# Performance work log

Measured on AMD Instinct MI355X. Metric: run time of the kernel, lower is better.

The kernel has to match this reference:

```python
import jax, jax.numpy as jnp
import numpy as np

CMIN, CMAX = -1024.0, 1016.0  # clamp(min=-2**10, max=2**10 - 8) after every op
BRIGHT_F = 1.9   # 1.0 + linspace(0, 0.9, 11)[10]
COLOR_F = 1.9    # 1.0 + linspace(0, 0.9, 11)[10]


def _brightness_dct(x, f):
    # pixel-domain multiplicative brightness; DCT is linear -> scale all coeffs
    return x * f


def _contrast_dct(x, f):
    # pixel contrast: (p - mean)*f + mean.
    # In DCT: AC coeffs scale by f; DC coeff blends toward per-channel mean DC.
    dc_mean = jnp.mean(x[..., 0, 0], axis=(-2, -1), keepdims=True)  # [C,1,1]
    out = x * f
    out = out.at[..., 0, 0].add((1.0 - f) * dc_mean)
    return out


def setup_inputs() -> dict:
    key = jax.random.key(0)
    k1, k2 = jax.random.split(key)
    # luma: [C=1, Hblocks, Wblocks, 8, 8]; chroma 4:2:0: [C=2, H/2, W/2, 8, 8]
    y = jax.random.normal(k1, (1, 512, 512, 8, 8), dtype=jnp.float32) * 100.0
    c = jax.random.normal(k2, (2, 256, 256, 8, 8), dtype=jnp.float32) * 100.0
    return {"y": y, "c": c}


def reference(y, c):
    clamp = lambda t: jnp.clip(t, CMIN, CMAX)
    # dct_prep(mode='start') treated as identity; initial clamp as in forward()
    y = clamp(y)
    c = clamp(c)
    # op 1: Brightness on luma (coeff[0]); both planes clamped after each op
    y = clamp(_brightness_dct(y, BRIGHT_F))
    c = clamp(c)
    # op 2: Color = contrast on chroma (coeff[1])
    c = clamp(_contrast_dct(c, COLOR_F))
    y = clamp(y)
    # dct_prep(mode='end') treated as identity
    return y, c
```

## Files before the change

### kernel.cpp

```cpp
#include <hip/hip_runtime.h>

#define CMIN -1024.0f
#define CMAX 1016.0f

__device__ __forceinline__ float clampv(float x) {
    return fminf(fmaxf(x, CMIN), CMAX);
}

__global__ void __launch_bounds__(256)
dc_sum_kernel(const float* __restrict__ c, float* __restrict__ ws,
              int dc_per_ch) {
    int t = blockIdx.x * blockDim.x + threadIdx.x;
    float v = clampv(c[(size_t)t * 64]);

    #pragma unroll
    for (int off = 32; off > 0; off >>= 1)
        v += __shfl_down(v, off, 64);

    __shared__ float smem[4];
    int lane = threadIdx.x & 63;
    int wave = threadIdx.x >> 6;
    if (lane == 0) smem[wave] = v;
    __syncthreads();
    if (threadIdx.x == 0) {
        float s = smem[0] + smem[1] + smem[2] + smem[3];
        int ch = (blockIdx.x * 256 < dc_per_ch) ? 0 : 1;
        atomicAdd(&ws[ch], s);
    }
}

__global__ void __launch_bounds__(256)
fused_elementwise(const float4* __restrict__ y, const float4* __restrict__ c,
                  float4* __restrict__ out, const float* __restrict__ ws,
                  int ynvec, int total_nvec, int c_half_nvec,
                  float inv_count) {
    int i = blockIdx.x * blockDim.x + threadIdx.x;
    if (i >= total_nvec) return;

    if (i < ynvec) {
        float4 v = y[i];
        v.x = clampv(clampv(v.x) * 1.9f);
        v.y = clampv(clampv(v.y) * 1.9f);
        v.z = clampv(clampv(v.z) * 1.9f);
        v.w = clampv(clampv(v.w) * 1.9f);
        out[i] = v;
    } else {
        int ci = i - ynvec;
        float4 v = c[ci];
        float4 r;
        r.x = clampv(v.x) * 1.9f;
        r.y = clampv(v.y) * 1.9f;
        r.z = clampv(v.z) * 1.9f;
        r.w = clampv(v.w) * 1.9f;
        if ((ci & 15) == 0) {
            int ch = (ci < c_half_nvec) ? 0 : 1;
            r.x += -0.9f * (ws[ch] * inv_count);
        }
        r.x = clampv(r.x);
        r.y = clampv(r.y);
        r.z = clampv(r.z);
        r.w = clampv(r.w);
        out[i] = r;
    }
}

extern "C" void kernel_launch(void* const* d_in, const int* in_sizes, int n_in,
                              void* d_out, int out_size, void* d_ws, size_t ws_size,
                              hipStream_t stream) {
    const float* y = (const float*)d_in[0];
    const float* c = (const float*)d_in[1];
    float* out = (float*)d_out;

    const int yN = in_sizes[0];
    const int cN = in_sizes[1];

    float* ws = (float*)d_ws;

    hipMemsetAsync(ws, 0, 2 * sizeof(float), stream);

    const int dc_count = cN / 64;
    const int dc_per_ch = dc_count / 2;
    dc_sum_kernel<<<dc_count / 256, 256, 0, stream>>>(c, ws, dc_per_ch);

    const int ynvec = yN / 4;
    const int cnvec = cN / 4;
    const int total_nvec = ynvec + cnvec;
    const float inv_count = 1.0f / (float)dc_per_ch;
    fused_elementwise<<<(total_nvec + 255) / 256, 256, 0, stream>>>(
        (const float4*)y, (const float4*)c, (float4*)out, ws,
        ynvec, total_nvec, cnvec / 2, inv_count);
}
```

Baseline: 183.7 us.

## Fuse DC reduction and elementwise pass into one persistent kernel with grid barrier

Merges the DC-sum kernel and the elementwise kernel into one persistent launch of 512 blocks. Each block adds its share of the chroma DC sum, processes the luma plane, then spins on an atomic counter until every block has contributed before processing chroma. This removes one kernel launch and hides the reduction behind the luma work. It relies on all 512 blocks being resident at once, or the spin-wait deadlocks, and it lowers the number of threads in flight compared with the one-thread-per-vector grid.

Result: slower. 202.8 us (+10.3%).

```diff
diff --git a/kernel.cpp b/kernel.cpp
--- a/kernel.cpp
+++ b/kernel.cpp
@@ -2,65 +2,78 @@
 
 #define CMIN -1024.0f
 #define CMAX 1016.0f
+#define NBLK 512
+#define NTHR 256
 
 __device__ __forceinline__ float clampv(float x) {
     return fminf(fmaxf(x, CMIN), CMAX);
 }
 
-__global__ void __launch_bounds__(256)
-dc_sum_kernel(const float* __restrict__ c, float* __restrict__ ws,
-              int dc_per_ch) {
-    int t = blockIdx.x * blockDim.x + threadIdx.x;
-    float v = clampv(c[(size_t)t * 64]);
+__global__ void __launch_bounds__(NTHR)
+fused_all(const float4* __restrict__ y4, const float4* __restrict__ c4,
+          const float*  __restrict__ c,  float4* __restrict__ outy,
+          float4* __restrict__ outc, float* __restrict__ ws,
+          unsigned* __restrict__ done,
+          int ynvec, int cnvec, int dc_per_ch, float inv_count) {
+    const int tid  = threadIdx.x;
+    const int gtid = blockIdx.x * NTHR + tid;
 
-    #pragma unroll
-    for (int off = 32; off > 0; off >>= 1)
-        v += __shfl_down(v, off, 64);
+    {
+        float v = clampv(c[(size_t)gtid * 64]);
+        #pragma unroll
+        for (int off = 32; off > 0; off >>= 1)
+            v += __shfl_down(v, off, 64);
+        __shared__ float smem[NTHR / 64];
+        if ((tid & 63) == 0) smem[tid >> 6] = v;
+        __syncthreads();
+        if (tid == 0) {
+            float s = 0.f;
+            #pragma unroll
+            for (int w = 0; w < NTHR / 64; ++w) s += smem[w];
+            const int ch = (gtid < dc_per_ch) ? 0 : 1;
+            atomicAdd(&ws[ch], s);
+            __threadfence();
+            atomicAdd(done, 1u);
+        }
+    }
 
-    __shared__ float smem[4];
-    int lane = threadIdx.x & 63;
-    int wave = threadIdx.x >> 6;
-    if (lane == 0) smem[wave] = v;
-    __syncthreads();
-    if (threadIdx.x == 0) {
-        float s = smem[0] + smem[1] + smem[2] + smem[3];
-        int ch = (blockIdx.x * 256 < dc_per_ch) ? 0 : 1;
-        atomicAdd(&ws[ch], s);
-    }
-}
-
-__global__ void __launch_bounds__(256)
-fused_elementwise(const float4* __restrict__ y, const float4* __restrict__ c,
-                  float4* __restrict__ out, const float* __restrict__ ws,
-                  int ynvec, int total_nvec, int c_half_nvec,
-                  float inv_count) {
-    int i = blockIdx.x * blockDim.x + threadIdx.x;
-    if (i >= total_nvec) return;
-
-    if (i < ynvec) {
-        float4 v = y[i];
+    for (int i = gtid; i < ynvec; i += NBLK * NTHR) {
+        float4 v = y4[i];
         v.x = clampv(clampv(v.x) * 1.9f);
         v.y = clampv(clampv(v.y) * 1.9f);
         v.z = clampv(clampv(v.z) * 1.9f);
         v.w = clampv(clampv(v.w) * 1.9f);
-        out[i] = v;
-    } else {
-        int ci = i - ynvec;
-        float4 v = c[ci];
+        outy[i] = v;
+    }
+
+    __shared__ float sdc[2];
+    if (tid == 0) {
+        while (__hip_atomic_load(done, __ATOMIC_ACQUIRE,
+                                 __HIP_MEMORY_SCOPE_AGENT) < (unsigned)NBLK) {}
+        sdc[0] = __hip_atomic_load(&ws[0], __ATOMIC_RELAXED,
+                                   __HIP_MEMORY_SCOPE_AGENT) * inv_count;
+        sdc[1] = __hip_atomic_load(&ws[1], __ATOMIC_RELAXED,
+                                   __HIP_MEMORY_SCOPE_AGENT) * inv_count;
+    }
+    __syncthreads();
+    const float adj0 = -0.9f * sdc[0];
+    const float adj1 = -0.9f * sdc[1];
+
+    const int chalf = cnvec >> 1;
+    for (int i = gtid; i < cnvec; i += NBLK * NTHR) {
+        float4 v = c4[i];
         float4 r;
         r.x = clampv(v.x) * 1.9f;
         r.y = clampv(v.y) * 1.9f;
         r.z = clampv(v.z) * 1.9f;
         r.w = clampv(v.w) * 1.9f;
-        if ((ci & 15) == 0) {
-            int ch = (ci < c_half_nvec) ? 0 : 1;
-            r.x += -0.9f * (ws[ch] * inv_count);
-        }
+        if ((i & 15) == 0)
+            r.x += (i < chalf) ? adj0 : adj1;
         r.x = clampv(r.x);
         r.y = clampv(r.y);
         r.z = clampv(r.z);
         r.w = clampv(r.w);
-        out[i] = r;
+        outc[i] = r;
     }
 }
 
@@ -75,18 +88,17 @@
     const int cN = in_sizes[1];
 
     float* ws = (float*)d_ws;
+    unsigned* done = (unsigned*)(ws + 2);
 
-    hipMemsetAsync(ws, 0, 2 * sizeof(float), stream);
-
-    const int dc_count = cN / 64;
-    const int dc_per_ch = dc_count / 2;
-    dc_sum_kernel<<<dc_count / 256, 256, 0, stream>>>(c, ws, dc_per_ch);
+    hipMemsetAsync(ws, 0, 16, stream);
 
     const int ynvec = yN / 4;
     const int cnvec = cN / 4;
-    const int total_nvec = ynvec + cnvec;
+    const int dc_per_ch = cN / 64 / 2;
     const float inv_count = 1.0f / (float)dc_per_ch;
-    fused_elementwise<<<(total_nvec + 255) / 256, 256, 0, stream>>>(
-        (const float4*)y, (const float4*)c, (float4*)out, ws,
-        ynvec, total_nvec, cnvec / 2, inv_count);
+
+    fused_all<<<NBLK, NTHR, 0, stream>>>(
+        (const float4*)y, (const float4*)c, c,
+        (float4*)out, (float4*)(out + yN),
+        ws, done, ynvec, cnvec, dc_per_ch, inv_count);
 }
```
